# Kernel optimization log

Hardware: AMD Instinct MI355X
Metric: run time of the kernel (lower is better)

The kernel has to match this reference:

```python
import jax, jax.numpy as jnp
import numpy as np
from jax import lax

PADLEN = 9  # 3 * max(len(a), len(b)) for an order-2 filter (3 taps each)


def _butter2_lowpass(cutoff, fs):
    # 2nd-order Butterworth lowpass via bilinear transform; matches
    # scipy.signal.butter(2, 2*cutoff/fs, btype='lowpass', output='ba')
    c = 1.0 / np.tan(np.pi * cutoff / fs)
    a0 = 1.0 + np.sqrt(2.0) * c + c * c
    b = np.array([1.0, 2.0, 1.0]) / a0
    a = np.array([a0, 2.0 - 2.0 * c * c, 1.0 - np.sqrt(2.0) * c + c * c]) / a0
    return b.astype(np.float32), a.astype(np.float32)


def setup_inputs() -> dict:
    key = jax.random.key(0)
    x = jax.random.normal(key, (16, 64, 48000), dtype=jnp.float32)
    b, a = _butter2_lowpass(1000.0, 48000.0)
    return {"x": x, "b": jnp.asarray(b), "a": jnp.asarray(a)}


def _pad_odd(x, n):
    # Odd-reflection padding, identical to _BaseFilter._pad_odd
    left_end = x[..., 0:1]
    left_ext = jnp.flip(x[..., 0:n], axis=-1)
    right_end = x[..., -1:]
    right_ext = jnp.flip(x[..., -(n + 2):-2], axis=-1)
    return jnp.concatenate((2.0 * left_end - left_ext, x, 2.0 * right_end - right_ext), axis=-1)


def _lfilter(x, a, b):
    # x: (N, T). Direct-form II transposed IIR with zero initial conditions
    # (same semantics as torchaudio.functional.lfilter, clamp=False).
    a0 = a[0]
    a_n = a / a0
    b_n = b / a0
    order = a.shape[0] - 1
    b0 = b_n[0]
    b_rest = b_n[1:]  # (order,)
    a_rest = a_n[1:]  # (order,)

    def step(z, xt):
        # z: (N, order) filter state, xt: (N,)
        y = b0 * xt + z[:, 0]
        z_new = xt[:, None] * b_rest - y[:, None] * a_rest
        z_new = z_new.at[:, :-1].add(z[:, 1:])
        return z_new, y

    z0 = jnp.zeros((x.shape[0], order), x.dtype)
    _, y = lax.scan(step, z0, x.T)  # y: (T, N)
    return y.T


def _filtfilt(x, a, b):
    # torchaudio.functional.filtfilt: forward lfilter (clamp=False), then
    # reversed lfilter with clamp=True (default), then reverse.
    fwd = _lfilter(x, a, b)
    bwd = _lfilter(jnp.flip(fwd, axis=-1), a, b)
    return jnp.clip(jnp.flip(bwd, axis=-1), -1.0, 1.0)


def reference(x, b, a):
    shape = x.shape
    scale = jnp.max(jnp.abs(x), axis=-1, keepdims=True)
    xn = x / scale
    xp = _pad_odd(xn, PADLEN)                     # (..., T + 2*PADLEN)
    x2 = xp.reshape(-1, xp.shape[-1])             # flatten lanes for the scan
    y2 = _filtfilt(x2, a, b)
    y = y2.reshape(shape[:-1] + (y2.shape[-1],))
    y = y[..., PADLEN:-PADLEN]                    # unpad back to T
    return y * scale
```

## Files before the change

### kernel.cpp

```cpp
#include <hip/hip_runtime.h>

#define NROWS 1024
#define N     48000
#define PAD   9
#define NPADE (N + PAD)

#define CL  32
#define W   (64 * CL)
#define WUL 3
#define WU  (WUL * CL)
#define MW  (W - 2 * WU)
#define NB  ((N + MW - 1) / MW)
#define NWIN (NB * NROWS)
#define WPB  4
#define NBLK (NWIN / WPB)

#define SWZ(g) (((g) & ~7) | (((g) & 7) ^ (((g) >> 3) & 7)))

__device__ __forceinline__ float xt_fetch(const float* __restrict__ xr, int t) {
    if (t < -PAD || t >= NPADE) return 0.0f;
    if (t < 0)  return 2.0f * xr[0]     - xr[-1 - t];
    if (t < N)  return xr[t];
    return 2.0f * xr[N - 1] - xr[2 * N - 3 - t];
}

#define FS(P, d) { float l0 = __shfl_up(s0, d), l1 = __shfl_up(s1, d);            \
    if (lane >= d) { s0 = fmaf(P.x, l0, fmaf(P.y, l1, s0));                       \
                     s1 = fmaf(P.z, l0, fmaf(P.w, l1, s1)); } }
#define BS(P, d) { float l0 = __shfl_down(s0, d), l1 = __shfl_down(s1, d);        \
    if (lane < 64 - d) { s0 = fmaf(P.x, l0, fmaf(P.y, l1, s0));                   \
                         s1 = fmaf(P.z, l0, fmaf(P.w, l1, s1)); } }

#define SQR() { float t00 = m00*m00 + m01*m10, t01 = m00*m01 + m01*m11;           \
                float t10 = m10*m00 + m11*m10, t11 = m10*m01 + m11*m11;           \
                m00 = t00; m01 = t01; m10 = t10; m11 = t11; }

__global__ __launch_bounds__(256, 4) void filt_kernel(
    const float* __restrict__ x,
    const float* __restrict__ bc,
    const float* __restrict__ ac,
    float* __restrict__ out)
{
    __shared__ float lds[WPB * W];

    const int lane = threadIdx.x & 63;
    const unsigned w = blockIdx.x * WPB + (threadIdx.x >> 6);
    const unsigned r = w / (unsigned)NB;
    const unsigned b = w - r * (unsigned)NB;
    const int R   = (int)b * MW;
    const int tb0 = R - WU;
    const int tb  = tb0 + lane * CL;

    const float b0 = bc[0], b1 = bc[1], b2 = bc[2];
    const float a1 = ac[1], a2 = ac[2];
    const float* xr = x + (size_t)r * N;
    float* wbuf = lds + (threadIdx.x >> 6) * W;

    float m00 = -a1, m01 = 1.f, m10 = -a2, m11 = 0.f;
    SQR() SQR() SQR() SQR() SQR()
    float4 P0 = make_float4(m00, m01, m10, m11); SQR()
    float4 P1 = make_float4(m00, m01, m10, m11); SQR()
    float4 P2 = make_float4(m00, m01, m10, m11); SQR()
    float4 P3 = make_float4(m00, m01, m10, m11); SQR()
    float4 P4 = make_float4(m00, m01, m10, m11); SQR()
    float4 P5 = make_float4(m00, m01, m10, m11);

    if (tb0 >= 0 && tb0 + W <= N) {
        const float4* src = (const float4*)(xr + tb0);
        #pragma unroll
        for (int m = 0; m < 8; ++m) {
            int l = m * 64 + lane;
            float4 v = src[l];
            *(float4*)(wbuf + 4 * SWZ(l)) = v;
        }
    } else {
        #pragma unroll
        for (int m = 0; m < 8; ++m) {
            int l = m * 64 + lane;
            int t = tb0 + 4 * l;
            float4 v = make_float4(xt_fetch(xr, t),     xt_fetch(xr, t + 1),
                                   xt_fetch(xr, t + 2), xt_fetch(xr, t + 3));
            *(float4*)(wbuf + 4 * SWZ(l)) = v;
        }
    }

    float c[CL];
    #pragma unroll
    for (int k = 0; k < 8; ++k) {
        float4 v = *(const float4*)(wbuf + 4 * (8 * lane + (k ^ (lane & 7))));
        int kk = 4 * k;
        c[kk] = v.x; c[kk+1] = v.y; c[kk+2] = v.z; c[kk+3] = v.w;
    }

    float z0 = 0.f, z1 = 0.f;
    #pragma unroll
    for (int k = 0; k < CL; ++k) {
        float xv = c[k];
        float y  = fmaf(b0, xv, z0);
        z0 = fmaf(-a1, y, fmaf(b1, xv, z1));
        z1 = fmaf(-a2, y, b2 * xv);
        c[k] = y;
    }

    float s0 = z0, s1 = z1;
    FS(P0, 1) FS(P1, 2) FS(P2, 4) FS(P3, 8) FS(P4, 16) FS(P5, 32)
    float in0 = __shfl_up(s0, 1), in1 = __shfl_up(s1, 1);
    if (lane == 0) { in0 = 0.f; in1 = 0.f; }

    float w0 = in0, w1 = in1;
    #pragma unroll
    for (int k = 0; k < CL; ++k) {
        c[k] += w0;
        float nw0 = fmaf(-a1, w0, w1);
        w1 = -a2 * w0;
        w0 = nw0;
    }

    if (tb + CL > NPADE) {
        #pragma unroll
        for (int k = 0; k < CL; ++k)
            if (tb + k >= NPADE) c[k] = 0.f;
    }

    z0 = 0.f; z1 = 0.f;
    #pragma unroll
    for (int k = CL - 1; k >= 0; --k) {
        float v = c[k];
        float y = fmaf(b0, v, z0);
        z0 = fmaf(-a1, y, fmaf(b1, v, z1));
        z1 = fmaf(-a2, y, b2 * v);
        c[k] = y;
    }

    s0 = z0; s1 = z1;
    BS(P0, 1) BS(P1, 2) BS(P2, 4) BS(P3, 8) BS(P4, 16) BS(P5, 32)
    in0 = __shfl_down(s0, 1); in1 = __shfl_down(s1, 1);
    if (lane == 63) { in0 = 0.f; in1 = 0.f; }

    w0 = in0; w1 = in1;
    #pragma unroll
    for (int k = CL - 1; k >= 0; --k) {
        c[k] += w0;
        float nw0 = fmaf(-a1, w0, w1);
        w1 = -a2 * w0;
        w0 = nw0;
    }

    #pragma unroll
    for (int k = 0; k < 8; ++k) {
        int kk = 4 * k;
        *(float4*)(wbuf + 4 * (8 * lane + (k ^ (lane & 7)))) =
            make_float4(c[kk], c[kk+1], c[kk+2], c[kk+3]);
    }

    float* orow = out + (size_t)r * N;
    #pragma unroll
    for (int m = 0; m < 8; ++m) {
        int l = m * 64 + lane;
        int t = tb0 + 4 * l;
        if (l >= WU / 4 && l < (WU + MW) / 4 && t + 4 <= N) {
            float4 v = *(const float4*)(wbuf + 4 * SWZ(l));
            *(float4*)(orow + t) = v;
        }
    }
}

extern "C" void kernel_launch(void* const* d_in, const int* in_sizes, int n_in,
                              void* d_out, int out_size, void* d_ws, size_t ws_size,
                              hipStream_t stream) {
    const float* x  = (const float*)d_in[0];
    const float* bc = (const float*)d_in[1];
    const float* ac = (const float*)d_in[2];
    float* out = (float*)d_out;

    filt_kernel<<<dim3(NBLK), dim3(256), 0, stream>>>(x, bc, ac, out);
}
```

Baseline: 80.21 us.

## Process two windows per wave with both global loads issued upfront

Each wave now handles a pair of adjacent windows in the same row and issues the global loads for both into registers before computing either one. The second window's load latency is meant to be hidden behind the first window's scan work. It also halves the wave count and the repeated coefficient-matrix setup. The cost is 32 more float4 registers per thread, which can lower occupancy. NB is hardcoded to 26, which matches the original ceiling division for these sizes.

```diff
diff --git a/kernel.cpp b/kernel.cpp
--- a/kernel.cpp
+++ b/kernel.cpp
@@ -10,10 +10,10 @@
 #define WUL 3
 #define WU  (WUL * CL)
 #define MW  (W - 2 * WU)
-#define NB  ((N + MW - 1) / MW)
-#define NWIN (NB * NROWS)
+#define NB  26
+#define NPAIR (NB / 2)
 #define WPB  4
-#define NBLK (NWIN / WPB)
+#define NBLK (NROWS * NPAIR / WPB)
 
 #define SWZ(g) (((g) & ~7) | (((g) & 7) ^ (((g) >> 3) & 7)))
 
@@ -35,54 +35,31 @@
                 float t10 = m10*m00 + m11*m10, t11 = m10*m01 + m11*m11;           \
                 m00 = t00; m01 = t01; m10 = t10; m11 = t11; }
 
-__global__ __launch_bounds__(256, 4) void filt_kernel(
-    const float* __restrict__ x,
-    const float* __restrict__ bc,
-    const float* __restrict__ ac,
-    float* __restrict__ out)
-{
-    __shared__ float lds[WPB * W];
-
-    const int lane = threadIdx.x & 63;
-    const unsigned w = blockIdx.x * WPB + (threadIdx.x >> 6);
-    const unsigned r = w / (unsigned)NB;
-    const unsigned b = w - r * (unsigned)NB;
-    const int R   = (int)b * MW;
-    const int tb0 = R - WU;
-    const int tb  = tb0 + lane * CL;
-
-    const float b0 = bc[0], b1 = bc[1], b2 = bc[2];
-    const float a1 = ac[1], a2 = ac[2];
-    const float* xr = x + (size_t)r * N;
-    float* wbuf = lds + (threadIdx.x >> 6) * W;
-
-    float m00 = -a1, m01 = 1.f, m10 = -a2, m11 = 0.f;
-    SQR() SQR() SQR() SQR() SQR()
-    float4 P0 = make_float4(m00, m01, m10, m11); SQR()
-    float4 P1 = make_float4(m00, m01, m10, m11); SQR()
-    float4 P2 = make_float4(m00, m01, m10, m11); SQR()
-    float4 P3 = make_float4(m00, m01, m10, m11); SQR()
-    float4 P4 = make_float4(m00, m01, m10, m11); SQR()
-    float4 P5 = make_float4(m00, m01, m10, m11);
-
+__device__ __forceinline__ void load_win(const float* __restrict__ xr, int tb0,
+                                         int lane, float4 (&h)[8]) {
     if (tb0 >= 0 && tb0 + W <= N) {
         const float4* src = (const float4*)(xr + tb0);
         #pragma unroll
-        for (int m = 0; m < 8; ++m) {
-            int l = m * 64 + lane;
-            float4 v = src[l];
-            *(float4*)(wbuf + 4 * SWZ(l)) = v;
-        }
+        for (int m = 0; m < 8; ++m) h[m] = src[m * 64 + lane];
     } else {
         #pragma unroll
         for (int m = 0; m < 8; ++m) {
-            int l = m * 64 + lane;
-            int t = tb0 + 4 * l;
-            float4 v = make_float4(xt_fetch(xr, t),     xt_fetch(xr, t + 1),
-                                   xt_fetch(xr, t + 2), xt_fetch(xr, t + 3));
-            *(float4*)(wbuf + 4 * SWZ(l)) = v;
+            int t = tb0 + 4 * (m * 64 + lane);
+            h[m] = make_float4(xt_fetch(xr, t),     xt_fetch(xr, t + 1),
+                               xt_fetch(xr, t + 2), xt_fetch(xr, t + 3));
         }
     }
+}
+
+__device__ __forceinline__ void process_window(
+    float4 (&h)[8], int tb0, int lane, float* __restrict__ wbuf,
+    float b0, float b1, float b2, float a1, float a2,
+    float4 P0, float4 P1, float4 P2, float4 P3, float4 P4, float4 P5,
+    float* __restrict__ orow)
+{
+    #pragma unroll
+    for (int m = 0; m < 8; ++m)
+        *(float4*)(wbuf + 4 * SWZ(m * 64 + lane)) = h[m];
 
     float c[CL];
     #pragma unroll
@@ -91,6 +68,7 @@
         int kk = 4 * k;
         c[kk] = v.x; c[kk+1] = v.y; c[kk+2] = v.z; c[kk+3] = v.w;
     }
+    const int tb = tb0 + lane * CL;
 
     float z0 = 0.f, z1 = 0.f;
     #pragma unroll
@@ -153,7 +131,6 @@
             make_float4(c[kk], c[kk+1], c[kk+2], c[kk+3]);
     }
 
-    float* orow = out + (size_t)r * N;
     #pragma unroll
     for (int m = 0; m < 8; ++m) {
         int l = m * 64 + lane;
@@ -163,6 +140,46 @@
             *(float4*)(orow + t) = v;
         }
     }
+}
+
+__global__ __launch_bounds__(256, 4) void filt_kernel(
+    const float* __restrict__ x,
+    const float* __restrict__ bc,
+    const float* __restrict__ ac,
+    float* __restrict__ out)
+{
+    __shared__ float lds[WPB * W];
+
+    const int lane = threadIdx.x & 63;
+    const unsigned u = blockIdx.x * WPB + (threadIdx.x >> 6);
+    const unsigned r = u / (unsigned)NPAIR;
+    const unsigned k = u - r * (unsigned)NPAIR;
+    const int tb0a = (int)(2 * k)     * MW - WU;
+    const int tb0b = (int)(2 * k + 1) * MW - WU;
+
+    const float b0 = bc[0], b1 = bc[1], b2 = bc[2];
+    const float a1 = ac[1], a2 = ac[2];
+    const float* xr = x + (size_t)r * N;
+    float* orow = out + (size_t)r * N;
+    float* wbuf = lds + (threadIdx.x >> 6) * W;
+
+    float m00 = -a1, m01 = 1.f, m10 = -a2, m11 = 0.f;
+    SQR() SQR() SQR() SQR() SQR()
+    float4 P0 = make_float4(m00, m01, m10, m11); SQR()
+    float4 P1 = make_float4(m00, m01, m10, m11); SQR()
+    float4 P2 = make_float4(m00, m01, m10, m11); SQR()
+    float4 P3 = make_float4(m00, m01, m10, m11); SQR()
+    float4 P4 = make_float4(m00, m01, m10, m11); SQR()
+    float4 P5 = make_float4(m00, m01, m10, m11);
+
+    float4 A[8], B[8];
+    load_win(xr, tb0a, lane, A);
+    load_win(xr, tb0b, lane, B);
+
+    process_window(A, tb0a, lane, wbuf, b0, b1, b2, a1, a2,
+                   P0, P1, P2, P3, P4, P5, orow);
+    process_window(B, tb0b, lane, wbuf, b0, b1, b2, a1, a2,
+                   P0, P1, P2, P3, P4, P5, orow);
 }
 
 extern "C" void kernel_launch(void* const* d_in, const int* in_sizes, int n_in,
```

Result: slower. 127.9 us (+59.5%).

## Halve per-wave LDS staging buffer and raise occupancy, scalarize filter coefficients

Applied to the files above, without the earlier changes.

Stages each 2048-sample window through LDS in two 1024-sample halves, so the shared-memory footprint per block halves and the launch bound rises to 8 blocks per CU. Filter coefficients and the scan matrix powers are moved into scalar registers with readfirstlane, which frees vector registers for the higher occupancy target. The two-phase staging adds serialization and divergent half-wave LDS reads and writes. Forcing 8 waves per SIMD could also cause register spills given the 32-element per-thread array.

```diff
diff --git a/kernel.cpp b/kernel.cpp
--- a/kernel.cpp
+++ b/kernel.cpp
@@ -6,16 +6,20 @@
 #define NPADE (N + PAD)
 
 #define CL  32
-#define W   (64 * CL)
-#define WUL 3
-#define WU  (WUL * CL)
-#define MW  (W - 2 * WU)
-#define NB  ((N + MW - 1) / MW)
-#define NWIN (NB * NROWS)
-#define WPB  4
-#define NBLK (NWIN / WPB)
+#define W   2048
+#define H   1024
+#define HG  256
+#define WU  96
+#define MW  1856
+#define NB  26
+#define WPB 4
+#define NBLK (NROWS * NB / WPB)
 
 #define SWZ(g) (((g) & ~7) | (((g) & 7) ^ (((g) >> 3) & 7)))
+
+__device__ __forceinline__ float rfl(float v) {
+    return __int_as_float(__builtin_amdgcn_readfirstlane(__float_as_int(v)));
+}
 
 __device__ __forceinline__ float xt_fetch(const float* __restrict__ xr, int t) {
     if (t < -PAD || t >= NPADE) return 0.0f;
@@ -24,72 +28,79 @@
     return 2.0f * xr[N - 1] - xr[2 * N - 3 - t];
 }
 
-#define FS(P, d) { float l0 = __shfl_up(s0, d), l1 = __shfl_up(s1, d);            \
-    if (lane >= d) { s0 = fmaf(P.x, l0, fmaf(P.y, l1, s0));                       \
-                     s1 = fmaf(P.z, l0, fmaf(P.w, l1, s1)); } }
-#define BS(P, d) { float l0 = __shfl_down(s0, d), l1 = __shfl_down(s1, d);        \
-    if (lane < 64 - d) { s0 = fmaf(P.x, l0, fmaf(P.y, l1, s0));                   \
-                         s1 = fmaf(P.z, l0, fmaf(P.w, l1, s1)); } }
+#define FS(px,py,pz,pw,d) { float l0 = __shfl_up(s0, d), l1 = __shfl_up(s1, d);   \
+    if (lane >= d) { s0 = fmaf(px, l0, fmaf(py, l1, s0));                         \
+                     s1 = fmaf(pz, l0, fmaf(pw, l1, s1)); } }
+#define BS(px,py,pz,pw,d) { float l0 = __shfl_down(s0, d), l1 = __shfl_down(s1, d);\
+    if (lane < 64 - d) { s0 = fmaf(px, l0, fmaf(py, l1, s0));                     \
+                         s1 = fmaf(pz, l0, fmaf(pw, l1, s1)); } }
 
 #define SQR() { float t00 = m00*m00 + m01*m10, t01 = m00*m01 + m01*m11;           \
                 float t10 = m10*m00 + m11*m10, t11 = m10*m01 + m11*m11;           \
                 m00 = t00; m01 = t01; m10 = t10; m11 = t11; }
 
-__global__ __launch_bounds__(256, 4) void filt_kernel(
+__global__ __launch_bounds__(256, 8) void filt_kernel(
     const float* __restrict__ x,
     const float* __restrict__ bc,
     const float* __restrict__ ac,
     float* __restrict__ out)
 {
-    __shared__ float lds[WPB * W];
+    __shared__ float lds[WPB * H];
 
     const int lane = threadIdx.x & 63;
-    const unsigned w = blockIdx.x * WPB + (threadIdx.x >> 6);
-    const unsigned r = w / (unsigned)NB;
-    const unsigned b = w - r * (unsigned)NB;
-    const int R   = (int)b * MW;
-    const int tb0 = R - WU;
+    const int wid  = threadIdx.x >> 6;
+    const unsigned w  = blockIdx.x * WPB + wid;
+    const unsigned r  = w / (unsigned)NB;
+    const unsigned wb = w - r * (unsigned)NB;
+    const int tb0 = (int)wb * MW - WU;
     const int tb  = tb0 + lane * CL;
 
-    const float b0 = bc[0], b1 = bc[1], b2 = bc[2];
-    const float a1 = ac[1], a2 = ac[2];
+    const float b0 = rfl(bc[0]), b1 = rfl(bc[1]), b2 = rfl(bc[2]);
+    const float a1 = rfl(ac[1]), a2 = rfl(ac[2]);
     const float* xr = x + (size_t)r * N;
-    float* wbuf = lds + (threadIdx.x >> 6) * W;
+    float* orow = out + (size_t)r * N;
+    float* wbuf = lds + wid * H;
 
     float m00 = -a1, m01 = 1.f, m10 = -a2, m11 = 0.f;
     SQR() SQR() SQR() SQR() SQR()
-    float4 P0 = make_float4(m00, m01, m10, m11); SQR()
-    float4 P1 = make_float4(m00, m01, m10, m11); SQR()
-    float4 P2 = make_float4(m00, m01, m10, m11); SQR()
-    float4 P3 = make_float4(m00, m01, m10, m11); SQR()
-    float4 P4 = make_float4(m00, m01, m10, m11); SQR()
-    float4 P5 = make_float4(m00, m01, m10, m11);
-
-    if (tb0 >= 0 && tb0 + W <= N) {
-        const float4* src = (const float4*)(xr + tb0);
-        #pragma unroll
-        for (int m = 0; m < 8; ++m) {
-            int l = m * 64 + lane;
-            float4 v = src[l];
-            *(float4*)(wbuf + 4 * SWZ(l)) = v;
-        }
-    } else {
-        #pragma unroll
-        for (int m = 0; m < 8; ++m) {
-            int l = m * 64 + lane;
-            int t = tb0 + 4 * l;
-            float4 v = make_float4(xt_fetch(xr, t),     xt_fetch(xr, t + 1),
-                                   xt_fetch(xr, t + 2), xt_fetch(xr, t + 3));
-            *(float4*)(wbuf + 4 * SWZ(l)) = v;
-        }
-    }
+    const float p0x=rfl(m00), p0y=rfl(m01), p0z=rfl(m10), p0w=rfl(m11); SQR()
+    const float p1x=rfl(m00), p1y=rfl(m01), p1z=rfl(m10), p1w=rfl(m11); SQR()
+    const float p2x=rfl(m00), p2y=rfl(m01), p2z=rfl(m10), p2w=rfl(m11); SQR()
+    const float p3x=rfl(m00), p3y=rfl(m01), p3z=rfl(m10), p3w=rfl(m11); SQR()
+    const float p4x=rfl(m00), p4y=rfl(m01), p4z=rfl(m10), p4w=rfl(m11); SQR()
+    const float p5x=rfl(m00), p5y=rfl(m01), p5z=rfl(m10), p5w=rfl(m11);
 
     float c[CL];
+
     #pragma unroll
-    for (int k = 0; k < 8; ++k) {
-        float4 v = *(const float4*)(wbuf + 4 * (8 * lane + (k ^ (lane & 7))));
-        int kk = 4 * k;
-        c[kk] = v.x; c[kk+1] = v.y; c[kk+2] = v.z; c[kk+3] = v.w;
+    for (int h = 0; h < 2; ++h) {
+        const int base = tb0 + h * H;
+        if (base >= 0 && base + H <= N) {
+            const float4* src = (const float4*)(xr + base);
+            #pragma unroll
+            for (int m = 0; m < 4; ++m) {
+                int g = m * 64 + lane;
+                *(float4*)(wbuf + 4 * SWZ(g)) = src[g];
+            }
+        } else {
+            #pragma unroll
+            for (int m = 0; m < 4; ++m) {
+                int g = m * 64 + lane;
+                int t = base + 4 * g;
+                *(float4*)(wbuf + 4 * SWZ(g)) =
+                    make_float4(xt_fetch(xr, t),     xt_fetch(xr, t + 1),
+                                xt_fetch(xr, t + 2), xt_fetch(xr, t + 3));
+            }
+        }
+        if ((lane >> 5) == h) {
+            const int j = lane & 31;
+            #pragma unroll
+            for (int k = 0; k < 8; ++k) {
+                float4 v = *(const float4*)(wbuf + 4 * (8 * j + (k ^ (j & 7))));
+                int kk = 4 * k;
+                c[kk] = v.x; c[kk+1] = v.y; c[kk+2] = v.z; c[kk+3] = v.w;
+            }
+        }
     }
 
     float z0 = 0.f, z1 = 0.f;
@@ -103,7 +114,8 @@
     }
 
     float s0 = z0, s1 = z1;
-    FS(P0, 1) FS(P1, 2) FS(P2, 4) FS(P3, 8) FS(P4, 16) FS(P5, 32)
+    FS(p0x,p0y,p0z,p0w, 1) FS(p1x,p1y,p1z,p1w, 2) FS(p2x,p2y,p2z,p2w, 4)
+    FS(p3x,p3y,p3z,p3w, 8) FS(p4x,p4y,p4z,p4w,16) FS(p5x,p5y,p5z,p5w,32)
     float in0 = __shfl_up(s0, 1), in1 = __shfl_up(s1, 1);
     if (lane == 0) { in0 = 0.f; in1 = 0.f; }
 
@@ -133,7 +145,8 @@
     }
 
     s0 = z0; s1 = z1;
-    BS(P0, 1) BS(P1, 2) BS(P2, 4) BS(P3, 8) BS(P4, 16) BS(P5, 32)
+    BS(p0x,p0y,p0z,p0w, 1) BS(p1x,p1y,p1z,p1w, 2) BS(p2x,p2y,p2z,p2w, 4)
+    BS(p3x,p3y,p3z,p3w, 8) BS(p4x,p4y,p4z,p4w,16) BS(p5x,p5y,p5z,p5w,32)
     in0 = __shfl_down(s0, 1); in1 = __shfl_down(s1, 1);
     if (lane == 63) { in0 = 0.f; in1 = 0.f; }
 
@@ -147,20 +160,24 @@
     }
 
     #pragma unroll
-    for (int k = 0; k < 8; ++k) {
-        int kk = 4 * k;
-        *(float4*)(wbuf + 4 * (8 * lane + (k ^ (lane & 7)))) =
-            make_float4(c[kk], c[kk+1], c[kk+2], c[kk+3]);
-    }
-
-    float* orow = out + (size_t)r * N;
-    #pragma unroll
-    for (int m = 0; m < 8; ++m) {
-        int l = m * 64 + lane;
-        int t = tb0 + 4 * l;
-        if (l >= WU / 4 && l < (WU + MW) / 4 && t + 4 <= N) {
-            float4 v = *(const float4*)(wbuf + 4 * SWZ(l));
-            *(float4*)(orow + t) = v;
+    for (int h = 0; h < 2; ++h) {
+        if ((lane >> 5) == h) {
+            const int j = lane & 31;
+            #pragma unroll
+            for (int k = 0; k < 8; ++k) {
+                int kk = 4 * k;
+                *(float4*)(wbuf + 4 * (8 * j + (k ^ (j & 7)))) =
+                    make_float4(c[kk], c[kk+1], c[kk+2], c[kk+3]);
+            }
+        }
+        const int base = tb0 + h * H;
+        #pragma unroll
+        for (int m = 0; m < 4; ++m) {
+            int g  = m * 64 + lane;
+            int gw = h * HG + g;
+            int t  = base + 4 * g;
+            if (gw >= WU / 4 && gw < (WU + MW) / 4 && t + 4 <= N)
+                *(float4*)(orow + t) = *(const float4*)(wbuf + 4 * SWZ(g));
         }
     }
 }
```

Measured after the change: 90.03 us. 1.12x slower.
